# Optimization experiments

Hardware: AMD Instinct MI355X
Metric: run time of the kernel (lower is better)

The kernel has to match this reference:

```python
import jax, jax.numpy as jnp
import numpy as np

NUM_HEADS = 16
FIELD_SIZE = 512
SIGMA = 3.0
EMB = 1024


def _causal_kernel_fft(G, sigma):
    # kernel[i] = exp(-|i - G//2| / sigma) for i < G//2, else 0; normalized
    i = np.arange(G)
    dist = np.abs(i - G // 2)
    kernel = np.where(i >= G // 2, 0.0, np.exp(-dist / sigma)).astype(np.float32)
    kernel = kernel / (kernel.sum() + 1e-8)
    return jnp.asarray(np.fft.rfft(kernel), dtype=jnp.complex64)


def setup_inputs() -> dict:
    key = jax.random.key(0)
    ks = jax.random.split(key, 9)
    B, N, D = 4, 4096, EMB
    s = 1.0 / np.sqrt(D)
    return {
        "x": jax.random.normal(ks[0], (B, N, D), dtype=jnp.float32),
        "q_w": jax.random.uniform(ks[1], (D, D), minval=-s, maxval=s, dtype=jnp.float32),
        "q_b": jnp.zeros((D,), jnp.float32),
        "k_w": jax.random.uniform(ks[2], (D, D), minval=-s, maxval=s, dtype=jnp.float32),
        "k_b": jnp.zeros((D,), jnp.float32),
        "v_w": jax.random.uniform(ks[3], (D, D), minval=-s, maxval=s, dtype=jnp.float32),
        "v_b": jnp.zeros((D,), jnp.float32),
        "out_w": jax.random.uniform(ks[4], (D, D), minval=-s, maxval=s, dtype=jnp.float32),
        "out_b": jnp.zeros((D,), jnp.float32),
    }


def reference(x, q_w, q_b, k_w, k_b, v_w, v_b, out_w, out_b):
    B, N, D = x.shape
    H, hd, G = NUM_HEADS, D // NUM_HEADS, FIELD_SIZE

    # projections (q is computed in the original but unused downstream)
    q = x @ q_w.T + q_b  # noqa: F841 (faithful to original)
    k = (x @ k_w.T + k_b).reshape(B, N, H, hd).transpose(0, 2, 1, 3)  # (B,H,N,hd)
    v = (x @ v_w.T + v_b).reshape(B, N, H, hd).transpose(0, 2, 1, 3)

    # map sequence positions -> field bins (same for all b, h)
    pos = jnp.arange(N, dtype=jnp.float32) / max(N - 1, 1) * (G - 1)
    field_idx = jnp.clip(pos.astype(jnp.int32), 0, G - 1)  # (N,)

    # weighted values by key magnitude
    k_mag = jnp.linalg.norm(k, axis=-1, keepdims=True)  # (B,H,N,1)
    wv = v * k_mag  # (B,H,N,hd)

    # scatter-add tokens into field bins (vectorized over B,H,hd)
    field = jax.ops.segment_sum(wv.transpose(2, 0, 1, 3), field_idx,
                                num_segments=G)  # (G,B,H,hd)
    field = field.transpose(1, 2, 0, 3)  # (B,H,G,hd)

    # causal convolution along the field via FFT (circular, as in original)
    kfft = _causal_kernel_fft(G, SIGMA)
    f_fft = jnp.fft.rfft(field, n=G, axis=2)
    conv = jnp.fft.irfft(f_fft * kfft[None, None, :, None], n=G, axis=2)

    # gather back to token positions
    out = conv[:, :, field_idx, :]  # (B,H,N,hd)
    out = out.transpose(0, 2, 1, 3).reshape(B, N, D)
    return out @ out_w.T + out_b
```

## Files before the change

### kernel.cpp

```cpp
#include <hip/hip_runtime.h>
#include <hip/hip_bf16.h>

#define NPOS 4096
#define DIM  1024
#define GSZ  512

#define GAS __attribute__((address_space(1)))
#define LAS __attribute__((address_space(3)))

typedef __attribute__((ext_vector_type(8))) short bf16x8;
typedef __attribute__((ext_vector_type(4))) float f32x4;

__device__ __forceinline__ void async_load16(const void* g, void* l) {
  __builtin_amdgcn_global_load_lds((const GAS void*)g, (LAS void*)l, 16, 0, 0);
}

__device__ __forceinline__ int fidx_of(int n) {
  return (int)(((float)n / 4095.0f) * 511.0f);
}

__device__ __forceinline__ float bf2f(unsigned short s) {
  union { unsigned u; float f; } v; v.u = ((unsigned)s) << 16; return v.f;
}

__device__ __forceinline__ void bin_range(int g, int& i0, int& i1) {
  i0 = (g * 4095 + 510) / 511;
  while (i0 > 0 && fidx_of(i0 - 1) >= g) --i0;
  while (i0 < NPOS && fidx_of(i0) < g) ++i0;
  if (g == GSZ - 1) { i1 = NPOS; return; }
  i1 = ((g + 1) * 4095 + 510) / 511;
  while (i1 > 0 && fidx_of(i1 - 1) >= g + 1) --i1;
  while (i1 < NPOS && fidx_of(i1) < g + 1) ++i1;
}

__global__ __launch_bounds__(256) void cast_all(
    const float* __restrict__ x, const float* __restrict__ kw,
    const float* __restrict__ vw, const float* __restrict__ ow,
    __hip_bfloat16* __restrict__ xb, __hip_bfloat16* __restrict__ kvwb,
    __hip_bfloat16* __restrict__ outwb) {
  int blk = blockIdx.x;
  const float* src; __hip_bfloat16* dst; int off;
  if (blk < 16384)      { src = x;  dst = xb;              off = blk; }
  else if (blk < 17408) { src = kw; dst = kvwb;            off = blk - 16384; }
  else if (blk < 18432) { src = vw; dst = kvwb + 1048576;  off = blk - 17408; }
  else                  { src = ow; dst = outwb;           off = blk - 18432; }
  int i = (off * 256 + threadIdx.x) * 4;
  float4 f = *(const float4*)(src + i);
  ushort4 o;
  __hip_bfloat16 t;
  t = __float2bfloat16(f.x); o.x = *(unsigned short*)&t;
  t = __float2bfloat16(f.y); o.y = *(unsigned short*)&t;
  t = __float2bfloat16(f.z); o.z = *(unsigned short*)&t;
  t = __float2bfloat16(f.w); o.w = *(unsigned short*)&t;
  *(ushort4*)(dst + i) = o;
}

__global__ __launch_bounds__(256) void gemm_bt(
    const __hip_bfloat16* __restrict__ A,
    const __hip_bfloat16* __restrict__ B,
    const float* __restrict__ bias0, const float* __restrict__ bias1,
    __hip_bfloat16* __restrict__ C, int N) {
  const int K = 1024;
  __shared__ __align__(16) __hip_bfloat16 As[128 * 32];
  __shared__ __align__(16) __hip_bfloat16 Bs[128 * 32];
  const int tid = threadIdx.x;
  const int bm = blockIdx.x * 128, bn = blockIdx.y * 128;

  const int srow = tid >> 2;
  const int scol = (tid & 3) * 8;
  const __hip_bfloat16* ap0 = A + (size_t)(bm + srow) * K + scol;
  const __hip_bfloat16* ap1 = A + (size_t)(bm + srow + 64) * K + scol;
  const __hip_bfloat16* bp0 = B + (size_t)(bn + srow) * K + scol;
  const __hip_bfloat16* bp1 = B + (size_t)(bn + srow + 64) * K + scol;
  __hip_bfloat16* as0 = &As[srow * 32 + scol];
  __hip_bfloat16* as1 = &As[(srow + 64) * 32 + scol];
  __hip_bfloat16* bs0 = &Bs[srow * 32 + scol];
  __hip_bfloat16* bs1 = &Bs[(srow + 64) * 32 + scol];

  const int wave = tid >> 6, lane = tid & 63;
  const int wm = (wave >> 1) * 64, wn = (wave & 1) * 64;
  const int m16 = lane & 15, quad = lane >> 4;

  f32x4 acc[4][4];
#pragma unroll
  for (int i = 0; i < 4; i++)
#pragma unroll
    for (int j = 0; j < 4; j++) acc[i][j] = (f32x4)0.f;

  for (int k0 = 0; k0 < K; k0 += 32) {
    async_load16(ap0 + k0, as0);
    async_load16(ap1 + k0, as1);
    async_load16(bp0 + k0, bs0);
    async_load16(bp1 + k0, bs1);
    __syncthreads();
    bf16x8 af[4], bfr[4];
#pragma unroll
    for (int mt = 0; mt < 4; mt++)
      af[mt] = *(const bf16x8*)&As[(wm + mt * 16 + m16) * 32 + quad * 8];
#pragma unroll
    for (int nt = 0; nt < 4; nt++)
      bfr[nt] = *(const bf16x8*)&Bs[(wn + nt * 16 + m16) * 32 + quad * 8];
#pragma unroll
    for (int mt = 0; mt < 4; mt++)
#pragma unroll
      for (int nt = 0; nt < 4; nt++)
        acc[mt][nt] = __builtin_amdgcn_mfma_f32_16x16x32_bf16(af[mt], bfr[nt], acc[mt][nt], 0, 0, 0);
    __syncthreads();
  }

#pragma unroll
  for (int mt = 0; mt < 4; mt++) {
#pragma unroll
    for (int nt = 0; nt < 4; nt++) {
      int col = bn + wn + nt * 16 + m16;
      float bv = (col < 1024) ? bias0[col] : bias1[col - 1024];
#pragma unroll
      for (int r = 0; r < 4; r++) {
        int row = bm + wm + mt * 16 + quad * 4 + r;
        C[(size_t)row * N + col] = __float2bfloat16(acc[mt][nt][r] + bv);
      }
    }
  }
}

__global__ __launch_bounds__(256) void gemm_out_bcast(
    const __hip_bfloat16* __restrict__ A,
    const __hip_bfloat16* __restrict__ B,
    const float* __restrict__ bias,
    float* __restrict__ out) {
  const int K = 1024;
  __shared__ __align__(16) __hip_bfloat16 As[64 * 32];
  __shared__ __align__(16) __hip_bfloat16 Bs[128 * 32];
  const int tid = threadIdx.x;
  const int bm = blockIdx.x * 64, bn = blockIdx.y * 128;

  const int srow = tid >> 2;
  const int scol = (tid & 3) * 8;
  const __hip_bfloat16* ap0 = A + (size_t)(bm + srow) * K + scol;
  const __hip_bfloat16* bp0 = B + (size_t)(bn + srow) * K + scol;
  const __hip_bfloat16* bp1 = B + (size_t)(bn + srow + 64) * K + scol;
  __hip_bfloat16* as0 = &As[srow * 32 + scol];
  __hip_bfloat16* bs0 = &Bs[srow * 32 + scol];
  __hip_bfloat16* bs1 = &Bs[(srow + 64) * 32 + scol];

  const int wave = tid >> 6, lane = tid & 63;
  const int wm = (wave >> 1) * 32, wn = (wave & 1) * 64;
  const int m16 = lane & 15, quad = lane >> 4;

  f32x4 acc[2][4];
#pragma unroll
  for (int i = 0; i < 2; i++)
#pragma unroll
    for (int j = 0; j < 4; j++) acc[i][j] = (f32x4)0.f;

  for (int k0 = 0; k0 < K; k0 += 32) {
    async_load16(ap0 + k0, as0);
    async_load16(bp0 + k0, bs0);
    async_load16(bp1 + k0, bs1);
    __syncthreads();
    bf16x8 af[2], bfr[4];
#pragma unroll
    for (int mt = 0; mt < 2; mt++)
      af[mt] = *(const bf16x8*)&As[(wm + mt * 16 + m16) * 32 + quad * 8];
#pragma unroll
    for (int nt = 0; nt < 4; nt++)
      bfr[nt] = *(const bf16x8*)&Bs[(wn + nt * 16 + m16) * 32 + quad * 8];
#pragma unroll
    for (int mt = 0; mt < 2; mt++)
#pragma unroll
      for (int nt = 0; nt < 4; nt++)
        acc[mt][nt] = __builtin_amdgcn_mfma_f32_16x16x32_bf16(af[mt], bfr[nt], acc[mt][nt], 0, 0, 0);
    __syncthreads();
  }

  float bv[4];
#pragma unroll
  for (int nt = 0; nt < 4; nt++) bv[nt] = bias[bn + wn + nt * 16 + m16];

#pragma unroll
  for (int mt = 0; mt < 2; mt++) {
#pragma unroll
    for (int r = 0; r < 4; r++) {
      int row = bm + wm + mt * 16 + quad * 4 + r;
      int b = row >> 9, g = row & (GSZ - 1);
      int i0, i1;
      bin_range(g, i0, i1);
      float v0 = acc[mt][0][r] + bv[0];
      float v1 = acc[mt][1][r] + bv[1];
      float v2 = acc[mt][2][r] + bv[2];
      float v3 = acc[mt][3][r] + bv[3];
      for (int n = i0; n < i1; ++n) {
        float* orow = out + ((size_t)(b * NPOS + n)) * DIM + bn + wn + m16;
        orow[0]  = v0;
        orow[16] = v1;
        orow[32] = v2;
        orow[48] = v3;
      }
    }
  }
}

__global__ __launch_bounds__(256) void wv_field_kernel(
    const __hip_bfloat16* __restrict__ KV, float* __restrict__ field) {
  const int b = blockIdx.x, g = blockIdx.y;
  int i0, i1;
  bin_range(g, i0, i1);
  int cnt = i1 - i0;
  if (cnt > 12) cnt = 12;
  __shared__ float km[12][16];
  const int tid = threadIdx.x;
  if (tid < cnt * 16) {
    int r = tid >> 4, h = tid & 15;
    const unsigned short* kp = (const unsigned short*)KV + (size_t)(b * NPOS + i0 + r) * 2048 + h * 64;
    float s = 0.f;
#pragma unroll
    for (int e = 0; e < 64; e += 8) {
      bf16x8 v = *(const bf16x8*)(kp + e);
#pragma unroll
      for (int q = 0; q < 8; ++q) { float f = bf2f((unsigned short)v[q]); s += f * f; }
    }
    km[r][h] = sqrtf(s);
  }
  __syncthreads();
  if (tid < 128) {
    int c0 = tid * 8, h = c0 >> 6;
    float acc[8] = {0.f, 0.f, 0.f, 0.f, 0.f, 0.f, 0.f, 0.f};
    for (int r = 0; r < cnt; ++r) {
      float w = km[r][h];
      bf16x8 v = *(const bf16x8*)((const unsigned short*)KV + (size_t)(b * NPOS + i0 + r) * 2048 + 1024 + c0);
#pragma unroll
      for (int q = 0; q < 8; ++q) acc[q] += w * bf2f((unsigned short)v[q]);
    }
    float4* fp = (float4*)(field + ((size_t)(b * GSZ + g)) * DIM + c0);
    fp[0] = make_float4(acc[0], acc[1], acc[2], acc[3]);
    fp[1] = make_float4(acc[4], acc[5], acc[6], acc[7]);
  }
}

__global__ __launch_bounds__(256) void conv_ema_kernel(
    const float* __restrict__ field, __hip_bfloat16* __restrict__ convb) {
  const int b = blockIdx.x, h = blockIdx.y;
  const int tid = threadIdx.x;
  const int c = tid & 63;
  const int chunk = blockIdx.z * 4 + (tid >> 6);
  const int n0 = chunk * 64;
  const float a = expf(-1.0f / 3.0f);
  const float w1 = 1.0f - a;
  const float* fb = field + (size_t)b * GSZ * DIM + h * 64 + c;
  float acc = 0.f;
#pragma unroll 4
  for (int n = n0 + 127; n >= n0 + 64; --n) {
    float f = fb[(size_t)((n + 257) & (GSZ - 1)) * DIM];
    acc = w1 * f + a * acc;
  }
#pragma unroll 4
  for (int n = n0 + 63; n >= n0; --n) {
    float f = fb[(size_t)((n + 257) & (GSZ - 1)) * DIM];
    acc = w1 * f + a * acc;
    convb[((size_t)(b * GSZ) + n) * DIM + h * 64 + c] = __float2bfloat16(acc);
  }
}

extern "C" void kernel_launch(void* const* d_in, const int* in_sizes, int n_in,
                              void* d_out, int out_size, void* d_ws, size_t ws_size,
                              hipStream_t stream) {
  (void)in_sizes; (void)n_in; (void)out_size; (void)ws_size;
  const float* x     = (const float*)d_in[0];
  const float* k_w   = (const float*)d_in[3];
  const float* k_b   = (const float*)d_in[4];
  const float* v_w   = (const float*)d_in[5];
  const float* v_b   = (const float*)d_in[6];
  const float* out_w = (const float*)d_in[7];
  const float* out_b = (const float*)d_in[8];

  char* p = (char*)d_ws;
  __hip_bfloat16* xb    = (__hip_bfloat16*)p; p += (size_t)16384 * 1024 * 2;
  __hip_bfloat16* kvwb  = (__hip_bfloat16*)p; p += (size_t)2048 * 1024 * 2;
  __hip_bfloat16* outwb = (__hip_bfloat16*)p; p += (size_t)1024 * 1024 * 2;
  __hip_bfloat16* KV    = (__hip_bfloat16*)p; p += (size_t)16384 * 2048 * 2;
  float*          field = (float*)p;          p += (size_t)4 * 512 * 1024 * 4;
  __hip_bfloat16* convb = (__hip_bfloat16*)p;

  cast_all<<<19456, 256, 0, stream>>>(x, k_w, v_w, out_w, xb, kvwb, outwb);

  gemm_bt<<<dim3(128, 16), 256, 0, stream>>>(xb, kvwb, k_b, v_b, KV, 2048);

  wv_field_kernel<<<dim3(4, 512), 256, 0, stream>>>(KV, field);
  conv_ema_kernel<<<dim3(4, 16, 2), 256, 0, stream>>>(field, convb);

  gemm_out_bcast<<<dim3(32, 8), 256, 0, stream>>>(convb, outwb, out_b, (float*)d_out);
}
```

Measured before the change: 283.5 us.

## Fuse key-norm into KV GEMM, stage conv in LDS, coalesce broadcast output stores

The KV GEMM epilogue now computes per-head key norms with lane shuffles and writes only V (bf16) plus a small norm array, so K is never written out. The field scatter kernel reads V and the precomputed norms, using all 256 threads. The EMA convolution stages a field slab in shared memory and launches more blocks. The output GEMM stages its tile in LDS and emits coalesced float4 row broadcasts instead of strided scalar stores, at the cost of extra LDS traffic and a block-wide sync.

```diff
diff --git a/kernel.cpp b/kernel.cpp
--- a/kernel.cpp
+++ b/kernel.cpp
@@ -55,11 +55,11 @@
   *(ushort4*)(dst + i) = o;
 }
 
-__global__ __launch_bounds__(256) void gemm_bt(
+__global__ __launch_bounds__(256) void gemm_kv(
     const __hip_bfloat16* __restrict__ A,
     const __hip_bfloat16* __restrict__ B,
-    const float* __restrict__ bias0, const float* __restrict__ bias1,
-    __hip_bfloat16* __restrict__ C, int N) {
+    const float* __restrict__ k_b, const float* __restrict__ v_b,
+    __hip_bfloat16* __restrict__ Vb, float* __restrict__ km) {
   const int K = 1024;
   __shared__ __align__(16) __hip_bfloat16 As[128 * 32];
   __shared__ __align__(16) __hip_bfloat16 Bs[128 * 32];
@@ -108,18 +108,92 @@
     __syncthreads();
   }
 
-#pragma unroll
-  for (int mt = 0; mt < 4; mt++) {
-#pragma unroll
-    for (int nt = 0; nt < 4; nt++) {
-      int col = bn + wn + nt * 16 + m16;
-      float bv = (col < 1024) ? bias0[col] : bias1[col - 1024];
+  if (bn < 1024) {
+    const int head = (bn + wn) >> 6;
+    float bv[4];
+#pragma unroll
+    for (int nt = 0; nt < 4; nt++) bv[nt] = k_b[bn + wn + nt * 16 + m16];
+#pragma unroll
+    for (int mt = 0; mt < 4; mt++) {
 #pragma unroll
       for (int r = 0; r < 4; r++) {
-        int row = bm + wm + mt * 16 + quad * 4 + r;
-        C[(size_t)row * N + col] = __float2bfloat16(acc[mt][nt][r] + bv);
+        float ss = 0.f;
+#pragma unroll
+        for (int nt = 0; nt < 4; nt++) {
+          float v = acc[mt][nt][r] + bv[nt];
+          ss += v * v;
+        }
+        ss += __shfl_xor(ss, 1);
+        ss += __shfl_xor(ss, 2);
+        ss += __shfl_xor(ss, 4);
+        ss += __shfl_xor(ss, 8);
+        if (m16 == 0) {
+          int row = bm + wm + mt * 16 + quad * 4 + r;
+          km[row * 16 + head] = sqrtf(ss);
+        }
       }
     }
+  } else {
+    float bv[4];
+#pragma unroll
+    for (int nt = 0; nt < 4; nt++) bv[nt] = v_b[bn + wn + nt * 16 + m16 - 1024];
+#pragma unroll
+    for (int mt = 0; mt < 4; mt++) {
+#pragma unroll
+      for (int nt = 0; nt < 4; nt++) {
+        int col = bn + wn + nt * 16 + m16 - 1024;
+#pragma unroll
+        for (int r = 0; r < 4; r++) {
+          int row = bm + wm + mt * 16 + quad * 4 + r;
+          Vb[(size_t)row * 1024 + col] = __float2bfloat16(acc[mt][nt][r] + bv[nt]);
+        }
+      }
+    }
+  }
+}
+
+__global__ __launch_bounds__(256) void wv_field_kernel(
+    const __hip_bfloat16* __restrict__ Vb, const float* __restrict__ km,
+    float* __restrict__ field) {
+  const int b = blockIdx.x, g = blockIdx.y;
+  int i0, i1;
+  bin_range(g, i0, i1);
+  const int tid = threadIdx.x;
+  const int c0 = tid * 4, h = tid >> 4;
+  float a0 = 0.f, a1 = 0.f, a2 = 0.f, a3 = 0.f;
+  for (int r = i0; r < i1; ++r) {
+    float w = km[(b * NPOS + r) * 16 + h];
+    ushort4 v = *(const ushort4*)((const unsigned short*)Vb + (size_t)(b * NPOS + r) * 1024 + c0);
+    a0 += w * bf2f(v.x); a1 += w * bf2f(v.y);
+    a2 += w * bf2f(v.z); a3 += w * bf2f(v.w);
+  }
+  *(float4*)(field + ((size_t)(b * GSZ + g)) * DIM + c0) = make_float4(a0, a1, a2, a3);
+}
+
+__global__ __launch_bounds__(256) void conv_ema_kernel(
+    const float* __restrict__ field, __hip_bfloat16* __restrict__ convb) {
+  const int b = blockIdx.x, h = blockIdx.y, n0 = blockIdx.z * 128;
+  __shared__ float slab[192 * 64];
+  const int tid = threadIdx.x;
+  const float* fb = field + (size_t)b * GSZ * DIM + h * 64;
+  for (int i = tid; i < 192 * 16; i += 256) {
+    int row = i >> 4, c4 = i & 15;
+    int gg = (n0 + 257 + row) & (GSZ - 1);
+    *(float4*)&slab[row * 64 + c4 * 4] = *(const float4*)(fb + (size_t)gg * DIM + c4 * 4);
+  }
+  __syncthreads();
+  const float a = 0.71653131057378927f;
+  const float w1 = 1.0f - a;
+  const int c = tid & 63, sub = tid >> 6;
+  const int e0 = sub * 32;
+  float acc = 0.f;
+#pragma unroll 4
+  for (int t = e0 + 95; t >= e0 + 32; --t)
+    acc = w1 * slab[t * 64 + c] + a * acc;
+#pragma unroll
+  for (int t = e0 + 31; t >= e0; --t) {
+    acc = w1 * slab[t * 64 + c] + a * acc;
+    convb[((size_t)(b * GSZ) + n0 + t) * DIM + h * 64 + c] = __float2bfloat16(acc);
   }
 }
 
@@ -129,8 +203,10 @@
     const float* __restrict__ bias,
     float* __restrict__ out) {
   const int K = 1024;
-  __shared__ __align__(16) __hip_bfloat16 As[64 * 32];
-  __shared__ __align__(16) __hip_bfloat16 Bs[128 * 32];
+  __shared__ __align__(16) char lds[64 * 132 * 4];
+  __hip_bfloat16* As = (__hip_bfloat16*)lds;
+  __hip_bfloat16* Bs = (__hip_bfloat16*)(lds + 4096);
+  float* Ct = (float*)lds;
   const int tid = threadIdx.x;
   const int bm = blockIdx.x * 64, bn = blockIdx.y * 128;
 
@@ -173,91 +249,32 @@
     __syncthreads();
   }
 
-  float bv[4];
-#pragma unroll
-  for (int nt = 0; nt < 4; nt++) bv[nt] = bias[bn + wn + nt * 16 + m16];
-
 #pragma unroll
   for (int mt = 0; mt < 2; mt++) {
 #pragma unroll
-    for (int r = 0; r < 4; r++) {
-      int row = bm + wm + mt * 16 + quad * 4 + r;
-      int b = row >> 9, g = row & (GSZ - 1);
-      int i0, i1;
-      bin_range(g, i0, i1);
-      float v0 = acc[mt][0][r] + bv[0];
-      float v1 = acc[mt][1][r] + bv[1];
-      float v2 = acc[mt][2][r] + bv[2];
-      float v3 = acc[mt][3][r] + bv[3];
-      for (int n = i0; n < i1; ++n) {
-        float* orow = out + ((size_t)(b * NPOS + n)) * DIM + bn + wn + m16;
-        orow[0]  = v0;
-        orow[16] = v1;
-        orow[32] = v2;
-        orow[48] = v3;
+    for (int nt = 0; nt < 4; nt++) {
+      int col = wn + nt * 16 + m16;
+      float bv = bias[bn + col];
+#pragma unroll
+      for (int r = 0; r < 4; r++) {
+        int row = wm + mt * 16 + quad * 4 + r;
+        Ct[row * 132 + col] = acc[mt][nt][r] + bv;
       }
     }
   }
-}
-
-__global__ __launch_bounds__(256) void wv_field_kernel(
-    const __hip_bfloat16* __restrict__ KV, float* __restrict__ field) {
-  const int b = blockIdx.x, g = blockIdx.y;
-  int i0, i1;
-  bin_range(g, i0, i1);
-  int cnt = i1 - i0;
-  if (cnt > 12) cnt = 12;
-  __shared__ float km[12][16];
-  const int tid = threadIdx.x;
-  if (tid < cnt * 16) {
-    int r = tid >> 4, h = tid & 15;
-    const unsigned short* kp = (const unsigned short*)KV + (size_t)(b * NPOS + i0 + r) * 2048 + h * 64;
-    float s = 0.f;
-#pragma unroll
-    for (int e = 0; e < 64; e += 8) {
-      bf16x8 v = *(const bf16x8*)(kp + e);
-#pragma unroll
-      for (int q = 0; q < 8; ++q) { float f = bf2f((unsigned short)v[q]); s += f * f; }
+  __syncthreads();
+
+  for (int gi = 0; gi < 64; ++gi) {
+    int R = bm + gi;
+    int b = R >> 9, g = R & (GSZ - 1);
+    int i0, i1;
+    bin_range(g, i0, i1);
+    int cnt = i1 - i0;
+    const float4* src = (const float4*)&Ct[gi * 132];
+    for (int it = tid; it < cnt * 32; it += 256) {
+      int n = i0 + (it >> 5), c4 = it & 31;
+      *(float4*)(out + ((size_t)(b * NPOS + n)) * DIM + bn + c4 * 4) = src[c4];
     }
-    km[r][h] = sqrtf(s);
-  }
-  __syncthreads();
-  if (tid < 128) {
-    int c0 = tid * 8, h = c0 >> 6;
-    float acc[8] = {0.f, 0.f, 0.f, 0.f, 0.f, 0.f, 0.f, 0.f};
-    for (int r = 0; r < cnt; ++r) {
-      float w = km[r][h];
-      bf16x8 v = *(const bf16x8*)((const unsigned short*)KV + (size_t)(b * NPOS + i0 + r) * 2048 + 1024 + c0);
-#pragma unroll
-      for (int q = 0; q < 8; ++q) acc[q] += w * bf2f((unsigned short)v[q]);
-    }
-    float4* fp = (float4*)(field + ((size_t)(b * GSZ + g)) * DIM + c0);
-    fp[0] = make_float4(acc[0], acc[1], acc[2], acc[3]);
-    fp[1] = make_float4(acc[4], acc[5], acc[6], acc[7]);
-  }
-}
-
-__global__ __launch_bounds__(256) void conv_ema_kernel(
-    const float* __restrict__ field, __hip_bfloat16* __restrict__ convb) {
-  const int b = blockIdx.x, h = blockIdx.y;
-  const int tid = threadIdx.x;
-  const int c = tid & 63;
-  const int chunk = blockIdx.z * 4 + (tid >> 6);
-  const int n0 = chunk * 64;
-  const float a = expf(-1.0f / 3.0f);
-  const float w1 = 1.0f - a;
-  const float* fb = field + (size_t)b * GSZ * DIM + h * 64 + c;
-  float acc = 0.f;
-#pragma unroll 4
-  for (int n = n0 + 127; n >= n0 + 64; --n) {
-    float f = fb[(size_t)((n + 257) & (GSZ - 1)) * DIM];
-    acc = w1 * f + a * acc;
-  }
-#pragma unroll 4
-  for (int n = n0 + 63; n >= n0; --n) {
-    float f = fb[(size_t)((n + 257) & (GSZ - 1)) * DIM];
-    acc = w1 * f + a * acc;
-    convb[((size_t)(b * GSZ) + n) * DIM + h * 64 + c] = __float2bfloat16(acc);
   }
 }
 
@@ -277,16 +294,17 @@
   __hip_bfloat16* xb    = (__hip_bfloat16*)p; p += (size_t)16384 * 1024 * 2;
   __hip_bfloat16* kvwb  = (__hip_bfloat16*)p; p += (size_t)2048 * 1024 * 2;
   __hip_bfloat16* outwb = (__hip_bfloat16*)p; p += (size_t)1024 * 1024 * 2;
-  __hip_bfloat16* KV    = (__hip_bfloat16*)p; p += (size_t)16384 * 2048 * 2;
+  __hip_bfloat16* Vb    = (__hip_bfloat16*)p; p += (size_t)16384 * 1024 * 2;
+  float*          km    = (float*)p;          p += (size_t)16384 * 16 * 4;
   float*          field = (float*)p;          p += (size_t)4 * 512 * 1024 * 4;
   __hip_bfloat16* convb = (__hip_bfloat16*)p;
 
   cast_all<<<19456, 256, 0, stream>>>(x, k_w, v_w, out_w, xb, kvwb, outwb);
 
-  gemm_bt<<<dim3(128, 16), 256, 0, stream>>>(xb, kvwb, k_b, v_b, KV, 2048);
-
-  wv_field_kernel<<<dim3(4, 512), 256, 0, stream>>>(KV, field);
-  conv_ema_kernel<<<dim3(4, 16, 2), 256, 0, stream>>>(field, convb);
+  gemm_kv<<<dim3(128, 16), 256, 0, stream>>>(xb, kvwb, k_b, v_b, Vb, km);
+
+  wv_field_kernel<<<dim3(4, 512), 256, 0, stream>>>(Vb, km, field);
+  conv_ema_kernel<<<dim3(4, 16, 4), 256, 0, stream>>>(field, convb);
 
   gemm_out_bcast<<<dim3(32, 8), 256, 0, stream>>>(convb, outwb, out_b, (float*)d_out);
 }
```

Result: slower. 349.7 us (+23.4%).
